# Optimization experiments

Measured on AMD Instinct MI355X. Metric: run time of the kernel, lower is better.

Reference implementation:

```python
import jax, jax.numpy as jnp
import numpy as np

EPS = 1e-6

def _ln(x):
    m = jnp.mean(x, -1, keepdims=True)
    v = jnp.mean((x - m) ** 2, -1, keepdims=True)
    return (x - m) * jax.lax.rsqrt(v + EPS)

def _rms(x, w):
    return x * jax.lax.rsqrt(jnp.mean(x * x, -1, keepdims=True) + EPS) * w

def _rotate_half(x):
    xr = x.reshape(x.shape[:-1] + (-1, 2))
    return jnp.stack([-xr[..., 1], xr[..., 0]], axis=-1).reshape(x.shape)

def _rope(x, cos, sin):
    # x: [B,L,H,D]; cos/sin: [L,D] interleaved-duplicated per pair
    c = cos[None, :, None, :]
    s = sin[None, :, None, :]
    return x * c + _rotate_half(x) * s

def _modulate(x, shift, scale):
    return x * (1.0 + scale[:, None, :]) + shift[:, None, :]

def _gate(x, g):
    return x * g[:, None, :]

def setup_inputs() -> dict:
    key = jax.random.key(0)
    ks = jax.random.split(key, 20)
    B, LI, LT, D, NH, HD, M = 1, 2048, 256, 2048, 16, 128, 8192
    def n(k, shape, s=1.0):
        return jax.random.normal(k, shape, dtype=jnp.float32) * s
    theta = jax.random.uniform(ks[0], (LI, HD // 2), dtype=jnp.float32) * 6.2831853
    freqs_cos = jnp.repeat(jnp.cos(theta), 2, axis=-1)  # [LI, HD]
    freqs_sin = jnp.repeat(jnp.sin(theta), 2, axis=-1)
    inp = {
        'img': n(ks[1], (B, LI, D)),
        'txt': n(ks[2], (B, LT, D)),
        'vec': n(ks[3], (B, D)),
        'freqs_cos': freqs_cos,
        'freqs_sin': freqs_sin,
        'attn_mask': jnp.ones((B, LI + LT), dtype=bool),
        # img stream params
        'img_mod_w': n(ks[4], (D, 6 * D), 0.02), 'img_mod_b': jnp.zeros((6 * D,), jnp.float32),
        'img_qkv_w': n(ks[5], (D, 3 * D), 0.02),
        'img_qn_w': jnp.ones((HD,), jnp.float32), 'img_kn_w': jnp.ones((HD,), jnp.float32),
        'img_proj_w': n(ks[6], (D, D), 0.02),
        'img_fc1_w': n(ks[7], (D, M), 0.02), 'img_fc1_b': jnp.zeros((M,), jnp.float32),
        'img_fc2_w': n(ks[8], (M, D), 0.02), 'img_fc2_b': jnp.zeros((D,), jnp.float32),
        # txt stream params
        'txt_mod_w': n(ks[9], (D, 6 * D), 0.02), 'txt_mod_b': jnp.zeros((6 * D,), jnp.float32),
        'txt_qkv_w': n(ks[10], (D, 3 * D), 0.02),
        'txt_qn_w': jnp.ones((HD,), jnp.float32), 'txt_kn_w': jnp.ones((HD,), jnp.float32),
        'txt_proj_w': n(ks[11], (D, D), 0.02),
        'txt_fc1_w': n(ks[12], (D, M), 0.02), 'txt_fc1_b': jnp.zeros((M,), jnp.float32),
        'txt_fc2_w': n(ks[13], (M, D), 0.02), 'txt_fc2_b': jnp.zeros((D,), jnp.float32),
    }
    return inp

def reference(img, txt, vec, freqs_cos, freqs_sin, attn_mask,
              img_mod_w, img_mod_b, img_qkv_w, img_qn_w, img_kn_w, img_proj_w,
              img_fc1_w, img_fc1_b, img_fc2_w, img_fc2_b,
              txt_mod_w, txt_mod_b, txt_qkv_w, txt_qn_w, txt_kn_w, txt_proj_w,
              txt_fc1_w, txt_fc1_b, txt_fc2_w, txt_fc2_b):
    B, LI, D = img.shape
    LT = txt.shape[1]
    HD = img_qn_w.shape[0]
    NH = D // HD
    vec_s = jax.nn.silu(vec)
    im = vec_s @ img_mod_w + img_mod_b
    i_s1, i_sc1, i_g1, i_s2, i_sc2, i_g2 = jnp.split(im, 6, axis=-1)
    tm = vec_s @ txt_mod_w + txt_mod_b
    t_s1, t_sc1, t_g1, t_s2, t_sc2, t_g2 = jnp.split(tm, 6, axis=-1)
    # img pre-attention
    ix = _modulate(_ln(img), i_s1, i_sc1)
    iqkv = (ix @ img_qkv_w).reshape(B, LI, 3, NH, HD)
    iq = _rms(iqkv[:, :, 0], img_qn_w)
    ik = _rms(iqkv[:, :, 1], img_kn_w)
    iv = iqkv[:, :, 2]
    iq = _rope(iq, freqs_cos, freqs_sin)
    ik = _rope(ik, freqs_cos, freqs_sin)
    # txt pre-attention (no rope)
    tx = _modulate(_ln(txt), t_s1, t_sc1)
    tqkv = (tx @ txt_qkv_w).reshape(B, LT, 3, NH, HD)
    tq = _rms(tqkv[:, :, 0], txt_qn_w)
    tk = _rms(tqkv[:, :, 1], txt_kn_w)
    tv = tqkv[:, :, 2]
    # joint attention over concat(img, txt)
    q = jnp.concatenate([iq, tq], axis=1)  # [B,S,H,D]
    k = jnp.concatenate([ik, tk], axis=1)
    v = jnp.concatenate([iv, tv], axis=1)
    scores = jnp.einsum('bqhd,bkhd->bhqk', q, k) / jnp.sqrt(jnp.float32(HD))
    scores = jnp.where(attn_mask[:, None, None, :], scores, jnp.float32(-1e30))
    p = jax.nn.softmax(scores, axis=-1)
    attn = jnp.einsum('bhqk,bkhd->bqhd', p, v).reshape(B, LI + LT, D)
    img_attn, txt_attn = attn[:, :LI], attn[:, LI:]
    # img residual branches
    img = img + _gate(img_attn @ img_proj_w, i_g1)
    h = _modulate(_ln(img), i_s2, i_sc2)
    h = jax.nn.gelu(h @ img_fc1_w + img_fc1_b, approximate=True) @ img_fc2_w + img_fc2_b
    img = img + _gate(h, i_g2)
    # txt residual branches
    txt = txt + _gate(txt_attn @ txt_proj_w, t_g1)
    h = _modulate(_ln(txt), t_s2, t_sc2)
    h = jax.nn.gelu(h @ txt_fc1_w + txt_fc1_b, approximate=True) @ txt_fc2_w + txt_fc2_b
    txt = txt + _gate(h, t_g2)
    return (img, txt)
```

## Files before the change

kernel.cpp:

```cpp
#include <hip/hip_runtime.h>
#include <hip/hip_bf16.h>
#include <cstdint>
#include <cstddef>

typedef __bf16 bf16x8 __attribute__((ext_vector_type(8)));
typedef float  f32x4  __attribute__((ext_vector_type(4)));
typedef __hip_bfloat16 hbf16;

#define DEVI static __device__ __forceinline__

DEVI unsigned short f2bf_bits(float x){
  hbf16 h = __float2bfloat16(x);
  return *reinterpret_cast<unsigned short*>(&h);
}
DEVI float gelu_tanh(float x){
  float u = x*(1.0f + 0.044715f*x*x);
  float t = exp2f(-2.3022119f*u);
  return x/(1.0f+t);
}

typedef __attribute__((address_space(1))) const unsigned int* gas_p;
typedef __attribute__((address_space(3))) unsigned int* las_p;
DEVI void gload16(const void* g, void* l){
  __builtin_amdgcn_global_load_lds((gas_p)g, (las_p)l, 16, 0, 0);
}


__global__ void silu_k(const float* __restrict__ v, float* __restrict__ o, int n){
  int i = blockIdx.x*blockDim.x + threadIdx.x;
  if (i < n){ float x = v[i]; o[i] = x/(1.0f+__expf(-x)); }
}

__global__ __launch_bounds__(256) void mod_part_k(const float* __restrict__ vs,
                                                  const float* __restrict__ W,
                                                  float* __restrict__ part){
  int j  = blockIdx.x*1024 + threadIdx.x*4;
  int i0 = blockIdx.y*64;
  float4 acc = {0.f,0.f,0.f,0.f};
  for (int i=0;i<64;i++){
    float s = vs[i0+i];
    float4 w = *(const float4*)(W + (size_t)(i0+i)*12288 + j);
    acc.x += s*w.x; acc.y += s*w.y; acc.z += s*w.z; acc.w += s*w.w;
  }
  *(float4*)(part + (size_t)blockIdx.y*12288 + j) = acc;
}

__global__ __launch_bounds__(256) void mod_red_k(const float* __restrict__ part,
                                                 const float* __restrict__ b,
                                                 float* __restrict__ out){
  int j = blockIdx.x*1024 + threadIdx.x*4;
  float4 acc = *(const float4*)(b + j);
  #pragma unroll
  for (int y=0;y<32;y++){
    float4 p = *(const float4*)(part + (size_t)y*12288 + j);
    acc.x += p.x; acc.y += p.y; acc.z += p.z; acc.w += p.w;
  }
  *(float4*)(out + j) = acc;
}

__global__ __launch_bounds__(256) void ln_mod_k(
    const float* __restrict__ Xi, const float* __restrict__ Xt,
    const float* __restrict__ sh_i, const float* __restrict__ sc_i,
    const float* __restrict__ sh_t, const float* __restrict__ sc_t,
    hbf16* __restrict__ Yi, hbf16* __restrict__ Yt){
  __shared__ float red[8];
  const int row = blockIdx.x, tid = threadIdx.x;
  const float* X; const float* sh; const float* sc; hbf16* Y; int r;
  if (row < 2048){ X = Xi; sh = sh_i; sc = sc_i; Y = Yi; r = row; }
  else           { X = Xt; sh = sh_t; sc = sc_t; Y = Yt; r = row - 2048; }
  const float* x = X + (size_t)r*2048;
  float4 a = *(const float4*)(x + tid*8);
  float4 c = *(const float4*)(x + tid*8 + 4);
  float s  = a.x+a.y+a.z+a.w + c.x+c.y+c.z+c.w;
  float s2 = a.x*a.x+a.y*a.y+a.z*a.z+a.w*a.w + c.x*c.x+c.y*c.y+c.z*c.z+c.w*c.w;
  #pragma unroll
  for (int m=1;m<64;m<<=1){ s += __shfl_xor(s,m,64); s2 += __shfl_xor(s2,m,64); }
  if ((tid&63)==0){ red[tid>>6] = s; red[4+(tid>>6)] = s2; }
  __syncthreads();
  float S  = red[0]+red[1]+red[2]+red[3];
  float S2 = red[4]+red[5]+red[6]+red[7];
  float mean = S*(1.f/2048.f);
  float var  = S2*(1.f/2048.f) - mean*mean;
  float rs = rsqrtf(var + 1e-6f);
  float xv[8] = {a.x,a.y,a.z,a.w,c.x,c.y,c.z,c.w};
  #pragma unroll
  for (int j=0;j<8;j++){
    int n = tid*8 + j;
    float yv = (xv[j]-mean)*rs*(1.f+sc[n]) + sh[n];
    Y[(size_t)r*2048 + n] = __float2bfloat16(yv);
  }
}

__global__ __launch_bounds__(256) void transp3_k(const float* __restrict__ W1,
                                                 hbf16* __restrict__ Wt1,
                                                 const float* __restrict__ W2,
                                                 hbf16* __restrict__ Wt2,
                                                 int K, int N){
  const float* W = blockIdx.z ? W2 : W1;
  hbf16* Wt = blockIdx.z ? Wt2 : Wt1;
  __shared__ float tile[128][68];
  const int n0 = blockIdx.x*64, k0 = blockIdx.y*128;
  const int tid = threadIdx.x;
  #pragma unroll
  for (int i=0;i<8;i++){
    int c = i*256 + tid;
    int k = c>>4, nq = c&15;
    float4 v = *(const float4*)(W + (size_t)(k0+k)*N + n0 + nq*4);
    *(float4*)&tile[k][nq*4] = v;
  }
  __syncthreads();
  const int n = tid>>2, kseg = tid&3;
  unsigned short buf[32];
  #pragma unroll
  for (int j=0;j<32;j++) buf[j] = f2bf_bits(tile[kseg*32+j][n]);
  hbf16* dst = Wt + (size_t)(n0+n)*K + k0 + kseg*32;
  *(uint4*)(dst)      = *(const uint4*)&buf[0];
  *(uint4*)(dst + 8)  = *(const uint4*)&buf[8];
  *(uint4*)(dst + 16) = *(const uint4*)&buf[16];
  *(uint4*)(dst + 24) = *(const uint4*)&buf[24];
}

__global__ __launch_bounds__(256) void vtransp_k(const hbf16* __restrict__ V,
                                                 hbf16* __restrict__ Vt){
  __shared__ unsigned short tile[64][72];
  const int t0 = blockIdx.x*64, d0 = blockIdx.y*64;
  const int tid = threadIdx.x;
  #pragma unroll
  for (int i=0;i<2;i++){
    int c = i*256 + tid, row = c>>3, jj = c&7;
    uint4 v = *(const uint4*)(V + (size_t)(t0+row)*2048 + d0 + jj*8);
    *(uint4*)&tile[row][jj*8] = v;
  }
  __syncthreads();
  const int d = tid>>2, seg = tid&3;
  unsigned short buf[16];
  #pragma unroll
  for (int j=0;j<16;j++) buf[j] = tile[seg*16+j][d];
  *(uint4*)(Vt + (size_t)(d0+d)*2304 + t0 + seg*16)     = *(const uint4*)&buf[0];
  *(uint4*)(Vt + (size_t)(d0+d)*2304 + t0 + seg*16 + 8) = *(const uint4*)&buf[8];
}

template<int EPI>
__global__ __launch_bounds__(256,2) void gemmbk_k(
    const hbf16* __restrict__ A1, const hbf16* __restrict__ B1,
    float* __restrict__ Cf1, const float* __restrict__ bias1,
    const float* __restrict__ gate1, const float* __restrict__ res1,
    const hbf16* __restrict__ A2, const hbf16* __restrict__ B2,
    float* __restrict__ Cf2, const float* __restrict__ bias2,
    const float* __restrict__ gate2, const float* __restrict__ res2,
    int nbx, int nby1, int nby2, int N, int K)
{
  __shared__ unsigned short As[128*128];
  __shared__ unsigned short Bs[128*128];
  const int tid = threadIdx.x;
  const int wv = tid>>6, ln = tid&63;
  const int nwg = nbx*(nby1+nby2), q = nwg>>3;
  const int w  = blockIdx.x;
  const int w2 = (w&7)*q + (w>>3);
  int n0, m0;
  const hbf16* A; const hbf16* Bt; float* Cf;
  const float* bias; const float* gate; const float* res;
  if (w2 < nbx*nby1){
    n0 = (w2/nby1)*128; m0 = (w2%nby1)*128;
    A=A1; Bt=B1; Cf=Cf1; bias=bias1; gate=gate1; res=res1;
  } else {
    int w3 = w2 - nbx*nby1;
    n0 = (w3/nby2)*128; m0 = (w3%nby2)*128;
    A=A2; Bt=B2; Cf=Cf2; bias=bias2; gate=gate2; res=res2;
  }
  const int wm = (wv>>1)*64, wn = (wv&1)*64;
  const int lm = ln&15, lk = ln>>4;
  f32x4 acc[4][4];
  #pragma unroll
  for (int i=0;i<4;i++)
    #pragma unroll
    for (int j=0;j<4;j++) acc[i][j] = (f32x4){0.f,0.f,0.f,0.f};

  const int srow = tid>>4;
  const int jsrc = (tid&15) ^ srow;
  const int NT = K>>7;

  for (int kt=0; kt<NT; ++kt){
    const int kk = kt<<7;
    #pragma unroll
    for (int i=0;i<8;i++){
      int row = i*16 + srow;
      gload16(A  + (size_t)(m0+row)*K + kk + jsrc*8, &As[(i*256+tid)*8]);
      gload16(Bt + (size_t)(n0+row)*K + kk + jsrc*8, &Bs[(i*256+tid)*8]);
    }
    __syncthreads();
    #pragma unroll
    for (int ks=0; ks<4; ++ks){
      bf16x8 af[4], bfv[4];
      #pragma unroll
      for (int qq=0;qq<4;qq++){
        int row = wm + qq*16 + lm;
        int jj  = ks*4 + lk;
        af[qq] = *(const bf16x8*)&As[row*128 + ((jj^(row&15))<<3)];
      }
      #pragma unroll
      for (int qq=0;qq<4;qq++){
        int row = wn + qq*16 + lm;
        int jj  = ks*4 + lk;
        bfv[qq] = *(const bf16x8*)&Bs[row*128 + ((jj^(row&15))<<3)];
      }
      #pragma unroll
      for (int i=0;i<4;i++)
        #pragma unroll
        for (int j=0;j<4;j++)
          acc[i][j] = __builtin_amdgcn_mfma_f32_16x16x32_bf16(af[i], bfv[j], acc[i][j], 0,0,0);
    }
    __syncthreads();
  }
  #pragma unroll
  for (int i=0;i<4;i++){
    int mbase = m0 + wm + i*16 + lk*4;
    #pragma unroll
    for (int j=0;j<4;j++){
      int n = n0 + wn + j*16 + lm;
      #pragma unroll
      for (int r=0;r<4;r++){
        size_t idx = (size_t)(mbase+r)*N + n;
        float v = acc[i][j][r];
        if constexpr (EPI==2){ Cf[idx] = res[idx] + gate[n]*v; }
        else { Cf[idx] = res[idx] + gate[n]*(v + bias[n]); }
      }
    }
  }
}

template<int EPI>
__global__ __launch_bounds__(512) void gemm256n_k(
    const hbf16* __restrict__ A1, const hbf16* __restrict__ B1,
    hbf16* __restrict__ Cb1, const float* __restrict__ bias1,
    const hbf16* __restrict__ A2, const hbf16* __restrict__ B2,
    hbf16* __restrict__ Cb2, const float* __restrict__ bias2,
    int nbx, int nby1, int nby2, int N, int K)
{
  __shared__ unsigned short As[256*64];
  __shared__ unsigned short Bs[128*64];
  const int tid = threadIdx.x;
  const int wv = tid>>6, ln = tid&63;
  const int nwg = nbx*(nby1+nby2), q = nwg>>3;
  const int w  = blockIdx.x;
  const int w2 = (w&7)*q + (w>>3);
  int n0, m0;
  const hbf16* A; const hbf16* Bt; hbf16* Cb; const float* bias;
  if (w2 < nbx*nby1){
    n0 = (w2/nby1)*128; m0 = (w2%nby1)*256;
    A=A1; Bt=B1; Cb=Cb1; bias=bias1;
  } else {
    int w3 = w2 - nbx*nby1;
    n0 = (w3/nby2)*128; m0 = (w3%nby2)*256;
    A=A2; Bt=B2; Cb=Cb2; bias=bias2;
  }
  const int wm = wv>>1, wn = wv&1;
  const int lm = ln&15, lk = ln>>4;
  f32x4 acc[4][4];
  #pragma unroll
  for (int i=0;i<4;i++)
    #pragma unroll
    for (int j=0;j<4;j++) acc[i][j] = (f32x4){0.f,0.f,0.f,0.f};

  const int srow = tid>>3;
  const int jsrc = (tid&7) ^ (srow&7);
  const int NT = K>>6;

  for (int kt=0; kt<NT; ++kt){
    const int kk = kt<<6;
    #pragma unroll
    for (int i=0;i<4;i++)
      gload16(A + (size_t)(m0 + i*64 + srow)*K + kk + jsrc*8, &As[(i*512+tid)*8]);
    #pragma unroll
    for (int i=0;i<2;i++)
      gload16(Bt + (size_t)(n0 + i*64 + srow)*K + kk + jsrc*8, &Bs[(i*512+tid)*8]);
    __syncthreads();
    #pragma unroll
    for (int ks=0; ks<2; ++ks){
      bf16x8 af[4], bfv[4];
      #pragma unroll
      for (int qq=0;qq<4;qq++){
        int row = wm*64 + qq*16 + lm;
        int jj  = ks*4 + lk;
        af[qq] = *(const bf16x8*)&As[row*64 + ((jj^(row&7))<<3)];
      }
      #pragma unroll
      for (int qq=0;qq<4;qq++){
        int row = wn*64 + qq*16 + lm;
        int jj  = ks*4 + lk;
        bfv[qq] = *(const bf16x8*)&Bs[row*64 + ((jj^(row&7))<<3)];
      }
      #pragma unroll
      for (int i=0;i<4;i++)
        #pragma unroll
        for (int j=0;j<4;j++)
          acc[i][j] = __builtin_amdgcn_mfma_f32_16x16x32_bf16(af[i], bfv[j], acc[i][j], 0,0,0);
    }
    __syncthreads();
  }
  #pragma unroll
  for (int i=0;i<4;i++){
    int mbase = m0 + wm*64 + i*16 + lk*4;
    #pragma unroll
    for (int j=0;j<4;j++){
      int n = n0 + wn*64 + j*16 + lm;
      #pragma unroll
      for (int r=0;r<4;r++){
        size_t idx = (size_t)(mbase+r)*N + n;
        float v = acc[i][j][r];
        if constexpr (EPI==1){ Cb[idx] = __float2bfloat16(gelu_tanh(v + bias[n])); }
        else { Cb[idx] = __float2bfloat16(v); }
      }
    }
  }
}

__global__ __launch_bounds__(512) void gemmqkv_k(
    const hbf16* __restrict__ A1, const hbf16* __restrict__ B1,
    const float* __restrict__ qn1, const float* __restrict__ kn1,
    int tok1, int rope1,
    const hbf16* __restrict__ A2, const hbf16* __restrict__ B2,
    const float* __restrict__ qn2, const float* __restrict__ kn2,
    int tok2, int rope2,
    const float* __restrict__ fcos_, const float* __restrict__ fsin_,
    hbf16* __restrict__ qb, hbf16* __restrict__ kb, hbf16* __restrict__ vb,
    int nbx, int nby1, int nby2, int K)
{
  __shared__ unsigned short As[256*64];
  __shared__ unsigned short Bs[128*64];
  __shared__ float ssb[2][256];
  const int tid = threadIdx.x;
  const int wv = tid>>6, ln = tid&63;
  const int nwg = nbx*(nby1+nby2), q = nwg>>3;
  const int w  = blockIdx.x;
  const int w2 = (w&7)*q + (w>>3);
  int n0, m0, tok, dorope;
  const hbf16* A; const hbf16* Bt; const float* qn; const float* kn;
  if (w2 < nbx*nby1){
    n0 = (w2/nby1)*128; m0 = (w2%nby1)*256;
    A=A1; Bt=B1; qn=qn1; kn=kn1; tok=tok1; dorope=rope1;
  } else {
    int w3 = w2 - nbx*nby1;
    n0 = (w3/nby2)*128; m0 = (w3%nby2)*256;
    A=A2; Bt=B2; qn=qn2; kn=kn2; tok=tok2; dorope=rope2;
  }
  const int wm = wv>>1, wn = wv&1;
  const int lm = ln&15, lk = ln>>4;
  f32x4 acc[4][4];
  #pragma unroll
  for (int i=0;i<4;i++)
    #pragma unroll
    for (int j=0;j<4;j++) acc[i][j] = (f32x4){0.f,0.f,0.f,0.f};

  const int srow = tid>>3;
  const int jsrc = (tid&7) ^ (srow&7);
  const int NT = K>>6;

  for (int kt=0; kt<NT; ++kt){
    const int kk = kt<<6;
    #pragma unroll
    for (int i=0;i<4;i++)
      gload16(A + (size_t)(m0 + i*64 + srow)*K + kk + jsrc*8, &As[(i*512+tid)*8]);
    #pragma unroll
    for (int i=0;i<2;i++)
      gload16(Bt + (size_t)(n0 + i*64 + srow)*K + kk + jsrc*8, &Bs[(i*512+tid)*8]);
    __syncthreads();
    #pragma unroll
    for (int ks=0; ks<2; ++ks){
      bf16x8 af[4], bfv[4];
      #pragma unroll
      for (int qq=0;qq<4;qq++){
        int row = wm*64 + qq*16 + lm;
        int jj  = ks*4 + lk;
        af[qq] = *(const bf16x8*)&As[row*64 + ((jj^(row&7))<<3)];
      }
      #pragma unroll
      for (int qq=0;qq<4;qq++){
        int row = wn*64 + qq*16 + lm;
        int jj  = ks*4 + lk;
        bfv[qq] = *(const bf16x8*)&Bs[row*64 + ((jj^(row&7))<<3)];
      }
      #pragma unroll
      for (int i=0;i<4;i++)
        #pragma unroll
        for (int j=0;j<4;j++)
          acc[i][j] = __builtin_amdgcn_mfma_f32_16x16x32_bf16(af[i], bfv[j], acc[i][j], 0,0,0);
    }
    __syncthreads();
  }

  const int which = n0 >> 11;
  const int head  = (n0 >> 7) & 15;
  if (which == 2){
    #pragma unroll
    for (int i=0;i<4;i++){
      int mbase = m0 + wm*64 + i*16 + lk*4;
      #pragma unroll
      for (int j=0;j<4;j++){
        int d = wn*64 + j*16 + lm;
        #pragma unroll
        for (int r=0;r<4;r++)
          vb[(size_t)(tok + mbase + r)*2048 + head*128 + d] = __float2bfloat16(acc[i][j][r]);
      }
    }
  } else {
    #pragma unroll
    for (int i=0;i<4;i++){
      #pragma unroll
      for (int r=0;r<4;r++){
        float p = 0.f;
        #pragma unroll
        for (int j=0;j<4;j++) p += acc[i][j][r]*acc[i][j][r];
        #pragma unroll
        for (int msk=1; msk<16; msk<<=1) p += __shfl_xor(p, msk, 64);
        if (lm == 0) ssb[wn][wm*64 + i*16 + lk*4 + r] = p;
      }
    }
    __syncthreads();
    const float* wgt = (which==0) ? qn : kn;
    const float qs = (which==0) ? 0.12751745f : 1.0f;
    hbf16* outb = (which==0) ? qb : kb;
    #pragma unroll
    for (int i=0;i<4;i++){
      #pragma unroll
      for (int r=0;r<4;r++){
        int row = wm*64 + i*16 + lk*4 + r;
        float ss = ssb[0][row] + ssb[1][row];
        float rs = rsqrtf(ss*(1.f/128.f) + 1e-6f) * qs;
        int t = m0 + row;
        #pragma unroll
        for (int j=0;j<4;j++){
          int d = wn*64 + j*16 + lm;
          float z = acc[i][j][r]*rs*wgt[d];
          float zp = __shfl_xor(z, 1, 64);
          float out;
          if (dorope){
            float c = fcos_[(size_t)t*128 + d];
            float s = fsin_[(size_t)t*128 + d];
            out = ((d&1)==0) ? (z*c - zp*s) : (z*c + zp*s);
          } else out = z;
          outb[(size_t)(tok + t)*2048 + head*128 + d] = __float2bfloat16(out);
        }
      }
    }
  }
}

__global__ __launch_bounds__(512,4) void attn_k(
    const hbf16* __restrict__ Qg, const hbf16* __restrict__ Kg,
    const hbf16* __restrict__ Vtg, hbf16* __restrict__ sop01,
    hbf16* __restrict__ sop23, float* __restrict__ mlp)
{
  const int w = blockIdx.x;
  const int h = w & 15, quarter = (w>>4)&3, q0 = (w>>6)*128;
  const int tid = threadIdx.x, wv = tid>>6, ln = tid&63;
  __shared__ unsigned short Ks[2][64*128];
  __shared__ unsigned short Vs[2][128*64];
  __shared__ unsigned short Ps[8][16*64];

  bf16x8 qf[4];
  {
    const hbf16* qrow = Qg + (size_t)(q0 + wv*16 + (ln&15))*2048 + h*128 + (ln>>4)*8;
    #pragma unroll
    for (int ks=0;ks<4;ks++) qf[ks] = *(const bf16x8*)(qrow + ks*32);
  }

  f32x4 so[8];
  #pragma unroll
  for (int i=0;i<8;i++) so[i] = (f32x4){0.f,0.f,0.f,0.f};
  float m_run[4] = {-3e38f,-3e38f,-3e38f,-3e38f};
  float l_run[4] = {0.f,0.f,0.f,0.f};

  auto stage = [&](int buf, int kt){
    const int k0 = kt*64;
    #pragma unroll
    for (int i=0;i<2;i++){
      int c = i*512 + tid;
      int row = c>>4, jj = c&15;
      int js = jj ^ (row&7);
      gload16(Kg + (size_t)(k0+row)*2048 + h*128 + js*8, &Ks[buf][(i*512 + wv*64)*8]);
    }
    #pragma unroll
    for (int i=0;i<2;i++){
      int c = i*512 + tid;
      int row = c>>3, jj = c&7;
      int js = jj ^ (row&7);
      gload16(Vtg + (size_t)(h*128+row)*2304 + k0 + js*8, &Vs[buf][(i*512 + wv*64)*8]);
    }
  };

  const int t0 = quarter*9;
  stage(0, t0);
  __syncthreads();

  for (int it=0; it<9; ++it){
    const int cur = it&1;
    if (it+1 < 9) stage(cur^1, t0+it+1);

    f32x4 s[4];
    #pragma unroll
    for (int nb=0;nb<4;nb++) s[nb] = (f32x4){0.f,0.f,0.f,0.f};
    __builtin_amdgcn_s_setprio(1);
    #pragma unroll
    for (int ks=0;ks<4;ks++){
      #pragma unroll
      for (int nb=0;nb<4;nb++){
        int rk = nb*16 + (ln&15);
        int jq = ks*4 + (ln>>4);
        bf16x8 bk = *(const bf16x8*)&Ks[cur][rk*128 + ((jq^(rk&7))<<3)];
        s[nb] = __builtin_amdgcn_mfma_f32_16x16x32_bf16(qf[ks], bk, s[nb], 0,0,0);
      }
    }
    __builtin_amdgcn_s_setprio(0);

    float scl[4];
    #pragma unroll
    for (int r=0;r<4;r++){
      float m1 = fmaxf(fmaxf(s[0][r], s[1][r]), fmaxf(s[2][r], s[3][r]));
      #pragma unroll
      for (int msk=1; msk<16; msk<<=1) m1 = fmaxf(m1, __shfl_xor(m1, msk, 64));
      float mn = fmaxf(m_run[r], m1);
      scl[r] = exp2f(m_run[r] - mn);
      m_run[r] = mn;
    }
    #pragma unroll
    for (int nb=0;nb<4;nb++)
      #pragma unroll
      for (int r=0;r<4;r++)
        s[nb][r] = exp2f(s[nb][r] - m_run[r]);
    #pragma unroll
    for (int r=0;r<4;r++){
      float sm = s[0][r]+s[1][r]+s[2][r]+s[3][r];
      #pragma unroll
      for (int msk=1; msk<16; msk<<=1) sm += __shfl_xor(sm, msk, 64);
      l_run[r] = l_run[r]*scl[r] + sm;
    }
    #pragma unroll
    for (int nb2=0;nb2<8;nb2++)
      #pragma unroll
      for (int r=0;r<4;r++) so[nb2][r] *= scl[r];

    #pragma unroll
    for (int nb=0;nb<4;nb++)
      #pragma unroll
      for (int r=0;r<4;r++){
        int m = ((ln>>4)<<2) + r;
        int n = nb*16 + (ln&15);
        Ps[wv][m*64 + (((n>>3)^(m&7))<<3) + (n&7)] = f2bf_bits(s[nb][r]);
      }

    __builtin_amdgcn_s_setprio(1);
    #pragma unroll
    for (int ks=0;ks<2;ks++){
      int mrow = ln&15;
      bf16x8 pa = *(const bf16x8*)&Ps[wv][mrow*64 + (((ks*4+(ln>>4))^(mrow&7))<<3)];
      #pragma unroll
      for (int nb2=0;nb2<8;nb2++){
        int rv = nb2*16 + (ln&15);
        int jv = ks*4 + (ln>>4);
        bf16x8 bv = *(const bf16x8*)&Vs[cur][rv*64 + ((jv^(rv&7))<<3)];
        so[nb2] = __builtin_amdgcn_mfma_f32_16x16x32_bf16(pa, bv, so[nb2], 0,0,0);
      }
    }
    __builtin_amdgcn_s_setprio(0);
    __syncthreads();
  }

  hbf16* sbase = (quarter < 2 ? sop01 + (size_t)quarter*2304*2048
                              : sop23 + (size_t)(quarter-2)*2304*2048);
  #pragma unroll
  for (int r=0;r<4;r++){
    int m = q0 + wv*16 + ((ln>>4)<<2) + r;
    #pragma unroll
    for (int nb2=0;nb2<8;nb2++){
      int d = h*128 + nb2*16 + (ln&15);
      sbase[(size_t)m*2048 + d] = __float2bfloat16(so[nb2][r]);
    }
  }
  if ((ln&15)==0){
    #pragma unroll
    for (int r=0;r<4;r++){
      int m = q0 + wv*16 + ((ln>>4)<<2) + r;
      float* p = mlp + ((size_t)(quarter*2304 + m)*16 + h)*2;
      p[0] = m_run[r]; p[1] = l_run[r];
    }
  }
}

__global__ __launch_bounds__(256) void amerge_k(const hbf16* __restrict__ sop01,
                                                const hbf16* __restrict__ sop23,
                                                const float* __restrict__ mlp,
                                                hbf16* __restrict__ Og){
  const int q = blockIdx.x, tid = threadIdx.x;
  const int d0 = tid*8, h = tid>>4;
  float mv[4], lv[4];
  float m = -3e38f;
  #pragma unroll
  for (int h4=0;h4<4;h4++){
    const float* p = mlp + ((size_t)(h4*2304 + q)*16 + h)*2;
    mv[h4] = p[0]; lv[h4] = p[1];
    m = fmaxf(m, mv[h4]);
  }
  float wgt[4], den = 0.f;
  #pragma unroll
  for (int h4=0;h4<4;h4++){ wgt[h4] = exp2f(mv[h4]-m); den += wgt[h4]*lv[h4]; }
  float inv = 1.0f/den;
  float acc[8] = {0,0,0,0,0,0,0,0};
  #pragma unroll
  for (int h4=0;h4<4;h4++){
    const hbf16* s = (h4<2 ? sop01 + (size_t)h4*2304*2048
                           : sop23 + (size_t)(h4-2)*2304*2048) + (size_t)q*2048 + d0;
    bf16x8 v = *(const bf16x8*)s;
    #pragma unroll
    for (int j=0;j<8;j++) acc[j] += wgt[h4]*(float)v[j];
  }
  hbf16* o = Og + (size_t)q*2048 + d0;
  #pragma unroll
  for (int j=0;j<8;j++) o[j] = __float2bfloat16(acc[j]*inv);
}


extern "C" void kernel_launch(void* const* d_in, const int* in_sizes, int n_in,
                              void* d_out, int out_size, void* d_ws, size_t ws_size,
                              hipStream_t stream) {
  (void)in_sizes; (void)n_in; (void)out_size; (void)ws_size;
  const float* img   = (const float*)d_in[0];
  const float* txt   = (const float*)d_in[1];
  const float* vec   = (const float*)d_in[2];
  const float* fcos  = (const float*)d_in[3];
  const float* fsin  = (const float*)d_in[4];
  const float* img_mod_w = (const float*)d_in[6];
  const float* img_mod_b = (const float*)d_in[7];
  const float* img_qkv_w = (const float*)d_in[8];
  const float* img_qn_w  = (const float*)d_in[9];
  const float* img_kn_w  = (const float*)d_in[10];
  const float* img_proj_w= (const float*)d_in[11];
  const float* img_fc1_w = (const float*)d_in[12];
  const float* img_fc1_b = (const float*)d_in[13];
  const float* img_fc2_w = (const float*)d_in[14];
  const float* img_fc2_b = (const float*)d_in[15];
  const float* txt_mod_w = (const float*)d_in[16];
  const float* txt_mod_b = (const float*)d_in[17];
  const float* txt_qkv_w = (const float*)d_in[18];
  const float* txt_qn_w  = (const float*)d_in[19];
  const float* txt_kn_w  = (const float*)d_in[20];
  const float* txt_proj_w= (const float*)d_in[21];
  const float* txt_fc1_w = (const float*)d_in[22];
  const float* txt_fc1_b = (const float*)d_in[23];
  const float* txt_fc2_w = (const float*)d_in[24];
  const float* txt_fc2_b = (const float*)d_in[25];

  float* out_img = (float*)d_out;
  float* out_txt = out_img + (size_t)2048*2048;

  char* ws = (char*)d_ws;
  size_t off = 0;
  auto alloc = [&](size_t bytes)->void*{
    void* p = ws + off; off += (bytes + 255) & ~(size_t)255; return p;
  };
  hbf16* wt1     = (hbf16*)alloc((size_t)16777216*2);
  hbf16* wt2     = (hbf16*)alloc((size_t)16777216*2);
  float* vs      = (float*)alloc(2048*4);
  float* im      = (float*)alloc(12288*4);
  float* tm      = (float*)alloc(12288*4);
  float* part    = (float*)alloc((size_t)2*32*12288*4);
  hbf16* ix      = (hbf16*)alloc((size_t)2048*2048*2);
  hbf16* tx      = (hbf16*)alloc((size_t)256*2048*2);
  hbf16* iqkvb   = (hbf16*)alloc((size_t)2048*6144*2);
  hbf16* tqkvb   = (hbf16*)alloc((size_t)256*6144*2);
  hbf16* qb      = (hbf16*)alloc((size_t)2304*2048*2);
  hbf16* kb      = (hbf16*)alloc((size_t)2304*2048*2);
  hbf16* vb      = (hbf16*)alloc((size_t)2304*2048*2);
  hbf16* vtg     = (hbf16*)alloc((size_t)2048*2304*2);
  hbf16* attnb   = (hbf16*)alloc((size_t)2304*2048*2);
  float* img_mid = (float*)alloc((size_t)2048*2048*4);
  float* txt_mid = (float*)alloc((size_t)256*2048*4);
  hbf16* ix2     = (hbf16*)alloc((size_t)2048*2048*2);
  hbf16* tx2     = (hbf16*)alloc((size_t)256*2048*2);
  hbf16* h1i     = (hbf16*)alloc((size_t)2048*8192*2);
  hbf16* h1t     = (hbf16*)alloc((size_t)256*8192*2);
  float* mlp     = (float*)alloc((size_t)4*2304*16*2*4);
  (void)iqkvb; (void)tqkvb;
  hbf16* sop01 = (hbf16*)ix;
  hbf16* sop23 = (hbf16*)img_mid;

  silu_k<<<8,256,0,stream>>>(vec, vs, 2048);
  mod_part_k<<<dim3(12,32),256,0,stream>>>(vs, img_mod_w, part);
  mod_part_k<<<dim3(12,32),256,0,stream>>>(vs, txt_mod_w, part + (size_t)32*12288);
  mod_red_k<<<12,256,0,stream>>>(part, img_mod_b, im);
  mod_red_k<<<12,256,0,stream>>>(part + (size_t)32*12288, txt_mod_b, tm);

  ln_mod_k<<<2304,256,0,stream>>>(img, txt, im+0, im+2048, tm+0, tm+2048, ix, tx);

  transp3_k<<<dim3(96,16,2),256,0,stream>>>(img_qkv_w, wt1, txt_qkv_w, wt2, 2048, 6144);
  gemmqkv_k<<<432,512,0,stream>>>(ix, wt1, img_qn_w, img_kn_w, 0, 1,
                                  tx, wt2, txt_qn_w, txt_kn_w, 2048, 0,
                                  fcos, fsin, qb, kb, vb,
                                  48, 8, 1, 2048);

  vtransp_k<<<dim3(36,32),256,0,stream>>>(vb, vtg);

  attn_k<<<1152,512,0,stream>>>(qb, kb, vtg, sop01, sop23, mlp);
  amerge_k<<<2304,256,0,stream>>>(sop01, sop23, mlp, attnb);

  transp3_k<<<dim3(32,16,2),256,0,stream>>>(img_proj_w, wt1, txt_proj_w, wt2, 2048, 2048);
  gemmbk_k<2><<<288,256,0,stream>>>(attnb, wt1, img_mid, nullptr, im+4096, img,
                                    attnb + (size_t)2048*2048, wt2, txt_mid, nullptr, tm+4096, txt,
                                    16, 16, 2, 2048, 2048);

  ln_mod_k<<<2304,256,0,stream>>>(img_mid, txt_mid, im+6144, im+8192, tm+6144, tm+8192, ix2, tx2);

  transp3_k<<<dim3(128,16,2),256,0,stream>>>(img_fc1_w, wt1, txt_fc1_w, wt2, 2048, 8192);
  gemm256n_k<1><<<576,512,0,stream>>>(ix2, wt1, h1i, img_fc1_b,
                                      tx2, wt2, h1t, txt_fc1_b,
                                      64, 8, 1, 8192, 2048);

  transp3_k<<<dim3(32,64,2),256,0,stream>>>(img_fc2_w, wt1, txt_fc2_w, wt2, 8192, 2048);
  gemmbk_k<3><<<288,256,0,stream>>>(h1i, wt1, out_img, img_fc2_b, im+10240, img_mid,
                                    h1t, wt2, out_txt, txt_fc2_b, tm+10240, txt_mid,
                                    16, 16, 2, 2048, 8192);
}
```

Before: 667.2 us.

## Fuse weight transposes into neighboring kernels via extra workgroups

Folds each weight transpose/bf16 conversion into an adjacent kernel launch as extra workgroups: the QKV transpose joins the first LayerNorm, the proj transpose joins the attention merge, and the fc1 transpose runs as extra blocks of a specialised proj GEMM. The workspace is rearranged so the transposed weights live in separate buffers and do not overwrite each other. This removes kernel launches and the serialisation between bandwidth-bound transposes and compute kernels, letting them overlap on the GPU. The cost is larger fused kernels with bigger shared-memory footprints, which can lower occupancy for the LN and merge parts, and a heavier workspace.

Result: no change. 674.6 us (+1.1%).

```diff
diff --git a/kernel.cpp b/kernel.cpp
--- a/kernel.cpp
+++ b/kernel.cpp
@@ -23,6 +23,28 @@
 typedef __attribute__((address_space(3))) unsigned int* las_p;
 DEVI void gload16(const void* g, void* l){
   __builtin_amdgcn_global_load_lds((gas_p)g, (las_p)l, 16, 0, 0);
+}
+
+DEVI void transp_body(const float* __restrict__ W, hbf16* __restrict__ Wt,
+                      int K, int N, int bx, int by, int tid, float (*tile)[68]){
+  const int n0 = bx*64, k0 = by*128;
+  #pragma unroll
+  for (int i=0;i<8;i++){
+    int c = i*256 + tid;
+    int k = c>>4, nq = c&15;
+    float4 v = *(const float4*)(W + (size_t)(k0+k)*N + n0 + nq*4);
+    *(float4*)&tile[k][nq*4] = v;
+  }
+  __syncthreads();
+  const int n = tid>>2, kseg = tid&3;
+  unsigned short buf[32];
+  #pragma unroll
+  for (int j=0;j<32;j++) buf[j] = f2bf_bits(tile[kseg*32+j][n]);
+  hbf16* dst = Wt + (size_t)(n0+n)*K + k0 + kseg*32;
+  *(uint4*)(dst)      = *(const uint4*)&buf[0];
+  *(uint4*)(dst + 8)  = *(const uint4*)&buf[8];
+  *(uint4*)(dst + 16) = *(const uint4*)&buf[16];
+  *(uint4*)(dst + 24) = *(const uint4*)&buf[24];
 }
 
 
@@ -58,17 +80,9 @@
   *(float4*)(out + j) = acc;
 }
 
-__global__ __launch_bounds__(256) void ln_mod_k(
-    const float* __restrict__ Xi, const float* __restrict__ Xt,
-    const float* __restrict__ sh_i, const float* __restrict__ sc_i,
-    const float* __restrict__ sh_t, const float* __restrict__ sc_t,
-    hbf16* __restrict__ Yi, hbf16* __restrict__ Yt){
-  __shared__ float red[8];
-  const int row = blockIdx.x, tid = threadIdx.x;
-  const float* X; const float* sh; const float* sc; hbf16* Y; int r;
-  if (row < 2048){ X = Xi; sh = sh_i; sc = sc_i; Y = Yi; r = row; }
-  else           { X = Xt; sh = sh_t; sc = sc_t; Y = Yt; r = row - 2048; }
-  const float* x = X + (size_t)r*2048;
+DEVI void ln_row(const float* __restrict__ x, const float* __restrict__ sh,
+                 const float* __restrict__ sc, hbf16* __restrict__ y,
+                 int tid, float* red){
   float4 a = *(const float4*)(x + tid*8);
   float4 c = *(const float4*)(x + tid*8 + 4);
   float s  = a.x+a.y+a.z+a.w + c.x+c.y+c.z+c.w;
@@ -86,9 +100,59 @@
   #pragma unroll
   for (int j=0;j<8;j++){
     int n = tid*8 + j;
-    float yv = (xv[j]-mean)*rs*(1.f+sc[n]) + sh[n];
-    Y[(size_t)r*2048 + n] = __float2bfloat16(yv);
-  }
+    y[n] = __float2bfloat16((xv[j]-mean)*rs*(1.f+sc[n]) + sh[n]);
+  }
+}
+
+__global__ __launch_bounds__(256) void ln_mod_k(
+    const float* __restrict__ Xi, const float* __restrict__ Xt,
+    const float* __restrict__ sh_i, const float* __restrict__ sc_i,
+    const float* __restrict__ sh_t, const float* __restrict__ sc_t,
+    hbf16* __restrict__ Yi, hbf16* __restrict__ Yt){
+  __shared__ float red[8];
+  const int row = blockIdx.x, tid = threadIdx.x;
+  if (row < 2048) ln_row(Xi + (size_t)row*2048, sh_i, sc_i, Yi + (size_t)row*2048, tid, red);
+  else            ln_row(Xt + (size_t)(row-2048)*2048, sh_t, sc_t, Yt + (size_t)(row-2048)*2048, tid, red);
+}
+
+__global__ __launch_bounds__(256) void lnqtr_k(
+    const float* __restrict__ Xi, const float* __restrict__ Xt,
+    const float* __restrict__ sh_i, const float* __restrict__ sc_i,
+    const float* __restrict__ sh_t, const float* __restrict__ sc_t,
+    hbf16* __restrict__ Yi, hbf16* __restrict__ Yt,
+    const float* __restrict__ Wq1, hbf16* __restrict__ Wtq1,
+    const float* __restrict__ Wq2, hbf16* __restrict__ Wtq2){
+  __shared__ float tile[128][68];
+  __shared__ float red[8];
+  const int w = blockIdx.x, tid = threadIdx.x;
+  if (w < 2304){
+    if (w < 2048) ln_row(Xi + (size_t)w*2048, sh_i, sc_i, Yi + (size_t)w*2048, tid, red);
+    else          ln_row(Xt + (size_t)(w-2048)*2048, sh_t, sc_t, Yt + (size_t)(w-2048)*2048, tid, red);
+  } else {
+    int idx = w - 2304;
+    int x = idx % 96, y = (idx/96) & 15, z = idx/1536;
+    transp_body(z ? Wq2 : Wq1, z ? Wtq2 : Wtq1, 2048, 6144, x, y, tid, tile);
+  }
+}
+
+__global__ __launch_bounds__(256) void vtransp_k(const hbf16* __restrict__ V,
+                                                 hbf16* __restrict__ Vt){
+  __shared__ unsigned short tile[64][72];
+  const int t0 = blockIdx.x*64, d0 = blockIdx.y*64;
+  const int tid = threadIdx.x;
+  #pragma unroll
+  for (int i=0;i<2;i++){
+    int c = i*256 + tid, row = c>>3, jj = c&7;
+    uint4 v = *(const uint4*)(V + (size_t)(t0+row)*2048 + d0 + jj*8);
+    *(uint4*)&tile[row][jj*8] = v;
+  }
+  __syncthreads();
+  const int d = tid>>2, seg = tid&3;
+  unsigned short buf[16];
+  #pragma unroll
+  for (int j=0;j<16;j++) buf[j] = tile[seg*16+j][d];
+  *(uint4*)(Vt + (size_t)(d0+d)*2304 + t0 + seg*16)     = *(const uint4*)&buf[0];
+  *(uint4*)(Vt + (size_t)(d0+d)*2304 + t0 + seg*16 + 8) = *(const uint4*)&buf[8];
 }
 
 __global__ __launch_bounds__(256) void transp3_k(const float* __restrict__ W1,
@@ -96,48 +160,9 @@
                                                  const float* __restrict__ W2,
                                                  hbf16* __restrict__ Wt2,
                                                  int K, int N){
-  const float* W = blockIdx.z ? W2 : W1;
-  hbf16* Wt = blockIdx.z ? Wt2 : Wt1;
   __shared__ float tile[128][68];
-  const int n0 = blockIdx.x*64, k0 = blockIdx.y*128;
-  const int tid = threadIdx.x;
-  #pragma unroll
-  for (int i=0;i<8;i++){
-    int c = i*256 + tid;
-    int k = c>>4, nq = c&15;
-    float4 v = *(const float4*)(W + (size_t)(k0+k)*N + n0 + nq*4);
-    *(float4*)&tile[k][nq*4] = v;
-  }
-  __syncthreads();
-  const int n = tid>>2, kseg = tid&3;
-  unsigned short buf[32];
-  #pragma unroll
-  for (int j=0;j<32;j++) buf[j] = f2bf_bits(tile[kseg*32+j][n]);
-  hbf16* dst = Wt + (size_t)(n0+n)*K + k0 + kseg*32;
-  *(uint4*)(dst)      = *(const uint4*)&buf[0];
-  *(uint4*)(dst + 8)  = *(const uint4*)&buf[8];
-  *(uint4*)(dst + 16) = *(const uint4*)&buf[16];
-  *(uint4*)(dst + 24) = *(const uint4*)&buf[24];
-}
-
-__global__ __launch_bounds__(256) void vtransp_k(const hbf16* __restrict__ V,
-                                                 hbf16* __restrict__ Vt){
-  __shared__ unsigned short tile[64][72];
-  const int t0 = blockIdx.x*64, d0 = blockIdx.y*64;
-  const int tid = threadIdx.x;
-  #pragma unroll
-  for (int i=0;i<2;i++){
-    int c = i*256 + tid, row = c>>3, jj = c&7;
-    uint4 v = *(const uint4*)(V + (size_t)(t0+row)*2048 + d0 + jj*8);
-    *(uint4*)&tile[row][jj*8] = v;
-  }
-  __syncthreads();
-  const int d = tid>>2, seg = tid&3;
-  unsigned short buf[16];
-  #pragma unroll
-  for (int j=0;j<16;j++) buf[j] = tile[seg*16+j][d];
-  *(uint4*)(Vt + (size_t)(d0+d)*2304 + t0 + seg*16)     = *(const uint4*)&buf[0];
-  *(uint4*)(Vt + (size_t)(d0+d)*2304 + t0 + seg*16 + 8) = *(const uint4*)&buf[8];
+  transp_body(blockIdx.z ? W2 : W1, blockIdx.z ? Wt2 : Wt1, K, N,
+              blockIdx.x, blockIdx.y, threadIdx.x, tile);
 }
 
 template<int EPI>
@@ -224,6 +249,101 @@
         float v = acc[i][j][r];
         if constexpr (EPI==2){ Cf[idx] = res[idx] + gate[n]*v; }
         else { Cf[idx] = res[idx] + gate[n]*(v + bias[n]); }
+      }
+    }
+  }
+}
+
+__global__ __launch_bounds__(256,2) void projtr_k(
+    const hbf16* __restrict__ A1, const hbf16* __restrict__ B1,
+    float* __restrict__ Cf1, const float* __restrict__ gate1,
+    const float* __restrict__ res1,
+    const hbf16* __restrict__ A2, const hbf16* __restrict__ B2,
+    float* __restrict__ Cf2, const float* __restrict__ gate2,
+    const float* __restrict__ res2,
+    const float* __restrict__ Wf1, hbf16* __restrict__ Wtf1,
+    const float* __restrict__ Wf2, hbf16* __restrict__ Wtf2)
+{
+  __shared__ __align__(16) unsigned char smem[65536];
+  const int tid = threadIdx.x;
+  const int w = blockIdx.x;
+  if (w >= 288){
+    int idx = w - 288;
+    int x = idx & 127, y = (idx>>7) & 15, z = idx>>11;
+    transp_body(z ? Wf2 : Wf1, z ? Wtf2 : Wtf1, 2048, 8192, x, y, tid,
+                (float(*)[68])smem);
+    return;
+  }
+  unsigned short* As = (unsigned short*)smem;
+  unsigned short* Bs = (unsigned short*)(smem + 32768);
+  const int wv = tid>>6, ln = tid&63;
+  const int nwg = 288, q = nwg>>3;
+  const int w2 = (w&7)*q + (w>>3);
+  int n0, m0;
+  const hbf16* A; const hbf16* Bt; float* Cf;
+  const float* gate; const float* res;
+  if (w2 < 256){
+    n0 = (w2/16)*128; m0 = (w2%16)*128;
+    A=A1; Bt=B1; Cf=Cf1; gate=gate1; res=res1;
+  } else {
+    int w3 = w2 - 256;
+    n0 = (w3/2)*128; m0 = (w3%2)*128;
+    A=A2; Bt=B2; Cf=Cf2; gate=gate2; res=res2;
+  }
+  const int wm = (wv>>1)*64, wn = (wv&1)*64;
+  const int lm = ln&15, lk = ln>>4;
+  f32x4 acc[4][4];
+  #pragma unroll
+  for (int i=0;i<4;i++)
+    #pragma unroll
+    for (int j=0;j<4;j++) acc[i][j] = (f32x4){0.f,0.f,0.f,0.f};
+
+  const int srow = tid>>4;
+  const int jsrc = (tid&15) ^ srow;
+  const int K = 2048, N = 2048, NT = K>>7;
+
+  for (int kt=0; kt<NT; ++kt){
+    const int kk = kt<<7;
+    #pragma unroll
+    for (int i=0;i<8;i++){
+      int row = i*16 + srow;
+      gload16(A  + (size_t)(m0+row)*K + kk + jsrc*8, &As[(i*256+tid)*8]);
+      gload16(Bt + (size_t)(n0+row)*K + kk + jsrc*8, &Bs[(i*256+tid)*8]);
+    }
+    __syncthreads();
+    #pragma unroll
+    for (int ks=0; ks<4; ++ks){
+      bf16x8 af[4], bfv[4];
+      #pragma unroll
+      for (int qq=0;qq<4;qq++){
+        int row = wm + qq*16 + lm;
+        int jj  = ks*4 + lk;
+        af[qq] = *(const bf16x8*)&As[row*128 + ((jj^(row&15))<<3)];
+      }
+      #pragma unroll
+      for (int qq=0;qq<4;qq++){
+        int row = wn + qq*16 + lm;
+        int jj  = ks*4 + lk;
+        bfv[qq] = *(const bf16x8*)&Bs[row*128 + ((jj^(row&15))<<3)];
+      }
+      #pragma unroll
+      for (int i=0;i<4;i++)
+        #pragma unroll
+        for (int j=0;j<4;j++)
+          acc[i][j] = __builtin_amdgcn_mfma_f32_16x16x32_bf16(af[i], bfv[j], acc[i][j], 0,0,0);
+    }
+    __syncthreads();
+  }
+  #pragma unroll
+  for (int i=0;i<4;i++){
+    int mbase = m0 + wm + i*16 + lk*4;
+    #pragma unroll
+    for (int j=0;j<4;j++){
+      int n = n0 + wn + j*16 + lm;
+      #pragma unroll
+      for (int r=0;r<4;r++){
+        size_t idx = (size_t)(mbase+r)*N + n;
+        Cf[idx] = res[idx] + gate[n]*acc[i][j][r];
       }
     }
   }
@@ -587,11 +707,20 @@
   }
 }
 
-__global__ __launch_bounds__(256) void amerge_k(const hbf16* __restrict__ sop01,
-                                                const hbf16* __restrict__ sop23,
-                                                const float* __restrict__ mlp,
-                                                hbf16* __restrict__ Og){
-  const int q = blockIdx.x, tid = threadIdx.x;
+__global__ __launch_bounds__(256) void amtr_k(
+    const hbf16* __restrict__ sop01, const hbf16* __restrict__ sop23,
+    const float* __restrict__ mlp, hbf16* __restrict__ Og,
+    const float* __restrict__ Wp1, hbf16* __restrict__ Wtp1,
+    const float* __restrict__ Wp2, hbf16* __restrict__ Wtp2){
+  __shared__ float tile[128][68];
+  const int w = blockIdx.x, tid = threadIdx.x;
+  if (w >= 2304){
+    int idx = w - 2304;
+    int x = idx & 31, y = (idx>>5) & 15, z = idx>>9;
+    transp_body(z ? Wp2 : Wp1, z ? Wtp2 : Wtp1, 2048, 2048, x, y, tid, tile);
+    return;
+  }
+  const int q = w;
   const int d0 = tid*8, h = tid>>4;
   float mv[4], lv[4];
   float m = -3e38f;
@@ -658,8 +787,15 @@
   auto alloc = [&](size_t bytes)->void*{
     void* p = ws + off; off += (bytes + 255) & ~(size_t)255; return p;
   };
-  hbf16* wt1     = (hbf16*)alloc((size_t)16777216*2);
-  hbf16* wt2     = (hbf16*)alloc((size_t)16777216*2);
+  hbf16* wblk    = (hbf16*)alloc((size_t)33554432*2);
+  hbf16* wtq1 = wblk;
+  hbf16* wtq2 = wblk + (size_t)2048*6144;
+  hbf16* wtp1 = wblk + (size_t)2*2048*6144;
+  hbf16* wtp2 = wtp1 + (size_t)2048*2048;
+  hbf16* wtf2_1 = wblk;
+  hbf16* wtf2_2 = wblk + (size_t)8192*2048;
+  hbf16* wtf1_1 = (hbf16*)alloc((size_t)2*8192*2048*2);
+  hbf16* wtf1_2 = wtf1_1 + (size_t)8192*2048;
   float* vs      = (float*)alloc(2048*4);
   float* im      = (float*)alloc(12288*4);
   float* tm      = (float*)alloc(12288*4);
@@ -690,33 +826,33 @@
   mod_red_k<<<12,256,0,stream>>>(part, img_mod_b, im);
   mod_red_k<<<12,256,0,stream>>>(part + (size_t)32*12288, txt_mod_b, tm);
 
-  ln_mod_k<<<2304,256,0,stream>>>(img, txt, im+0, im+2048, tm+0, tm+2048, ix, tx);
-
-  transp3_k<<<dim3(96,16,2),256,0,stream>>>(img_qkv_w, wt1, txt_qkv_w, wt2, 2048, 6144);
-  gemmqkv_k<<<432,512,0,stream>>>(ix, wt1, img_qn_w, img_kn_w, 0, 1,
-                                  tx, wt2, txt_qn_w, txt_kn_w, 2048, 0,
+  lnqtr_k<<<5376,256,0,stream>>>(img, txt, im+0, im+2048, tm+0, tm+2048, ix, tx,
+                                 img_qkv_w, wtq1, txt_qkv_w, wtq2);
+
+  gemmqkv_k<<<432,512,0,stream>>>(ix, wtq1, img_qn_w, img_kn_w, 0, 1,
+                                  tx, wtq2, txt_qn_w, txt_kn_w, 2048, 0,
                                   fcos, fsin, qb, kb, vb,
                                   48, 8, 1, 2048);
 
   vtransp_k<<<dim3(36,32),256,0,stream>>>(vb, vtg);
 
   attn_k<<<1152,512,0,stream>>>(qb, kb, vtg, sop01, sop23, mlp);
-  amerge_k<<<2304,256,0,stream>>>(sop01, sop23, mlp, attnb);
-
-  transp3_k<<<dim3(32,16,2),256,0,stream>>>(img_proj_w, wt1, txt_proj_w, wt2, 2048, 2048);
-  gemmbk_k<2><<<288,256,0,stream>>>(attnb, wt1, img_mid, nullptr, im+4096, img,
-                                    attnb + (size_t)2048*2048, wt2, txt_mid, nullptr, tm+4096, txt,
-                                    16, 16, 2, 2048, 2048);
+  amtr_k<<<3328,256,0,stream>>>(sop01, sop23, mlp, attnb,
+                                img_proj_w, wtp1, txt_proj_w, wtp2);
+
+  projtr_k<<<4384,256,0,stream>>>(attnb, wtp1, img_mid, im+4096, img,
+                                  attnb + (size_t)2048*2048, wtp2, txt_mid, tm+4096, txt,
+                                  img_fc1_w, wtf1_1, txt_fc1_w, wtf1_2);
 
   ln_mod_k<<<2304,256,0,stream>>>(img_mid, txt_mid, im+6144, im+8192, tm+6144, tm+8192, ix2, tx2);
 
-  transp3_k<<<dim3(128,16,2),256,0,stream>>>(img_fc1_w, wt1, txt_fc1_w, wt2, 2048, 8192);
-  gemm256n_k<1><<<576,512,0,stream>>>(ix2, wt1, h1i, img_fc1_b,
-                                      tx2, wt2, h1t, txt_fc1_b,
+  gemm256n_k<1><<<576,512,0,stream>>>(ix2, wtf1_1, h1i, img_fc1_b,
+                                      tx2, wtf1_2, h1t, txt_fc1_b,
                                       64, 8, 1, 8192, 2048);
 
-  transp3_k<<<dim3(32,64,2),256,0,stream>>>(img_fc2_w, wt1, txt_fc2_w, wt2, 8192, 2048);
-  gemmbk_k<3><<<288,256,0,stream>>>(h1i, wt1, out_img, img_fc2_b, im+10240, img_mid,
-                                    h1t, wt2, out_txt, txt_fc2_b, tm+10240, txt_mid,
+  transp3_k<<<dim3(32,64,2),256,0,stream>>>(img_fc2_w, wtf2_1, txt_fc2_w, wtf2_2, 8192, 2048);
+
+  gemmbk_k<3><<<288,256,0,stream>>>(h1i, wtf2_1, out_img, img_fc2_b, im+10240, img_mid,
+                                    h1t, wtf2_2, out_txt, txt_fc2_b, tm+10240, txt_mid,
                                     16, 16, 2, 2048, 8192);
 }
```
